# Kernel tuning notes

Hardware: AMD Instinct MI355X
Metric: run time of the kernel (lower is better)

## Reference

```python
import jax, jax.numpy as jnp
import numpy as np

B, L, H = 32, 4096, 512


def setup_inputs() -> dict:
    key = jax.random.key(0)
    k1, k2, k3, k4 = jax.random.split(key, 4)
    hidden = jax.random.normal(k1, (2, 2, B, H), dtype=jnp.float32)  # (h/c, layers, batch, H)
    encoder_outputs = jax.random.normal(k2, (B, L, H), dtype=jnp.float32)
    W = jax.random.normal(k3, (H, H), dtype=jnp.float32) * (1.0 / np.sqrt(H))
    b = jax.random.normal(k4, (H,), dtype=jnp.float32) * 0.02
    return {"hidden": hidden, "encoder_outputs": encoder_outputs, "W": W, "b": b}


def reference(hidden, encoder_outputs, W, b):
    # hidden[0]: h-state [layers, batch, H] -> transpose(0,1) -> [batch, layers, H] -> last layer
    h_last = hidden[0].transpose(1, 0, 2)[:, -1, :]            # [B, H]
    # method == 'general': energy[b,i] = h_last[b] . (W @ enc[b,i] + b)
    proj = jnp.einsum('blh,oh->blo', encoder_outputs, W) + b   # [B, L, H]
    energies = jnp.einsum('bh,blh->bl', h_last, proj)          # [B, L]
    return jax.nn.softmax(energies, axis=1)[:, None, :]        # [B, 1, L]
```

## Files before the change

kernel.cpp:

```cpp
#include <hip/hip_runtime.h>

#define BATCH 32
#define LSEQ 4096
#define HDIM 512

typedef float f32x4 __attribute__((ext_vector_type(4)));

__global__ __launch_bounds__(512) void proj_kernel(
    const float* __restrict__ hidden, const float* __restrict__ W,
    const float* __restrict__ bias, float* __restrict__ vpart,
    float* __restrict__ cpart)
{
    const int b    = blockIdx.x;
    const int part = blockIdx.y;
    const int h    = threadIdx.x;
    const int obase = part * (HDIM / 2);

    __shared__ float s_hl[HDIM / 2];
    if (h < HDIM / 2) s_hl[h] = hidden[(BATCH + b) * HDIM + obase + h];
    __syncthreads();

    float acc = 0.f;
#pragma unroll 16
    for (int o = 0; o < HDIM / 2; ++o) {
        acc += s_hl[o] * W[(obase + o) * HDIM + h];
    }
    vpart[(part * BATCH + b) * HDIM + h] = acc;

    float p = (h < HDIM / 2) ? s_hl[h] * bias[obase + h] : 0.f;
#pragma unroll
    for (int off = 1; off < 64; off <<= 1) p += __shfl_xor(p, off, 64);

    __shared__ float red[8];
    const int wid  = h >> 6;
    const int lane = h & 63;
    if (lane == 0) red[wid] = p;
    __syncthreads();
    if (h == 0) {
        float s = 0.f;
#pragma unroll
        for (int w = 0; w < 8; ++w) s += red[w];
        cpart[part * BATCH + b] = s;
    }
}

__global__ __launch_bounds__(256) void energy_kernel(
    const float* __restrict__ enc, const float* __restrict__ vA,
    const float* __restrict__ vB, const float* __restrict__ cA,
    const float* __restrict__ cB, float* __restrict__ energies)
{
    const int wave = threadIdx.x >> 6;
    const int lane = threadIdx.x & 63;
    const long r0 = (long)blockIdx.x * 16 + wave * 4;
    const int b = (int)(r0 >> 12);

    const f32x4* e4 = (const f32x4*)(enc + r0 * HDIM) + lane * 2;
    const float4* va = (const float4*)(vA + (long)b * HDIM) + lane * 2;
    const float4* vb = (const float4*)(vB + (long)b * HDIM) + lane * 2;

    f32x4 e[8];
#pragma unroll
    for (int j = 0; j < 4; ++j) {
        e[2 * j]     = __builtin_nontemporal_load(e4 + j * 128);
        e[2 * j + 1] = __builtin_nontemporal_load(e4 + j * 128 + 1);
    }
    float4 v0 = va[0], v1 = va[1];
    const float4 w0 = vb[0], w1 = vb[1];
    v0.x += w0.x; v0.y += w0.y; v0.z += w0.z; v0.w += w0.w;
    v1.x += w1.x; v1.y += w1.y; v1.z += w1.z; v1.w += w1.w;

    float d[4];
#pragma unroll
    for (int j = 0; j < 4; ++j) {
        const f32x4 a = e[2 * j], c = e[2 * j + 1];
        d[j] = a.x * v0.x + a.y * v0.y + a.z * v0.z + a.w * v0.w
             + c.x * v1.x + c.y * v1.y + c.z * v1.z + c.w * v1.w;
    }

#pragma unroll
    for (int off = 1; off < 64; off <<= 1) {
#pragma unroll
        for (int j = 0; j < 4; ++j) d[j] += __shfl_xor(d[j], off, 64);
    }

    if (lane == 0) {
        const float cb = cA[b] + cB[b];
        float4 out = { d[0] + cb, d[1] + cb, d[2] + cb, d[3] + cb };
        *(float4*)(energies + r0) = out;
    }
}

__global__ __launch_bounds__(512) void softmax_kernel(float* __restrict__ out)
{
    const int b = blockIdx.x;
    const int t = threadIdx.x;
    const int wid  = t >> 6;
    const int lane = t & 63;

    float4* o4 = (float4*)(out + (long)b * LSEQ);

    float4 v0 = o4[t], v1 = o4[512 + t];
    float m = fmaxf(fmaxf(fmaxf(v0.x, v0.y), fmaxf(v0.z, v0.w)),
                    fmaxf(fmaxf(v1.x, v1.y), fmaxf(v1.z, v1.w)));

    __shared__ float smax[8];
#pragma unroll
    for (int off = 1; off < 64; off <<= 1) m = fmaxf(m, __shfl_xor(m, off, 64));
    if (lane == 0) smax[wid] = m;
    __syncthreads();
#pragma unroll
    for (int w = 0; w < 8; ++w) m = fmaxf(m, smax[w]);

    v0.x = __expf(v0.x - m); v0.y = __expf(v0.y - m);
    v0.z = __expf(v0.z - m); v0.w = __expf(v0.w - m);
    v1.x = __expf(v1.x - m); v1.y = __expf(v1.y - m);
    v1.z = __expf(v1.z - m); v1.w = __expf(v1.w - m);

    float s = v0.x + v0.y + v0.z + v0.w + v1.x + v1.y + v1.z + v1.w;
    __shared__ float ssum[8];
#pragma unroll
    for (int off = 1; off < 64; off <<= 1) s += __shfl_xor(s, off, 64);
    if (lane == 0) ssum[wid] = s;
    __syncthreads();
    s = 0.f;
#pragma unroll
    for (int w = 0; w < 8; ++w) s += ssum[w];

    const float inv = 1.0f / s;
    v0.x *= inv; v0.y *= inv; v0.z *= inv; v0.w *= inv;
    v1.x *= inv; v1.y *= inv; v1.z *= inv; v1.w *= inv;
    o4[t] = v0;
    o4[512 + t] = v1;
}

extern "C" void kernel_launch(void* const* d_in, const int* in_sizes, int n_in,
                              void* d_out, int out_size, void* d_ws, size_t ws_size,
                              hipStream_t stream)
{
    const float* hidden = (const float*)d_in[0];
    const float* enc    = (const float*)d_in[1];
    const float* W      = (const float*)d_in[2];
    const float* bias   = (const float*)d_in[3];

    float* ws    = (float*)d_ws;
    float* vpart = ws;
    float* cpart = ws + 2 * BATCH * HDIM;

    float* out = (float*)d_out;

    proj_kernel<<<dim3(BATCH, 2), 512, 0, stream>>>(hidden, W, bias, vpart, cpart);
    energy_kernel<<<(BATCH * LSEQ) / 16, 256, 0, stream>>>(
        enc, vpart, vpart + BATCH * HDIM, cpart, cpart + BATCH, out);
    softmax_kernel<<<BATCH, 512, 0, stream>>>(out);
}
```

Measured before the change: 61.29 us.

## Split projection into four parts and restructure energy kernel with per-row subgroups

The projection kernel now splits the output dimension into four parts instead of two, giving more blocks and a shorter serial loop per thread. The energy kernel is restructured so each wave handles 32 rows, with 16-lane subgroups per row, a 4-step shuffle reduction, and the projected vector loaded once per thread and reused across rows. The softmax uses 1024 threads with one float4 each. The aim is to cut redundant vector loads and long shuffle chains in the bandwidth-bound energy pass, at the cost of fewer blocks in flight and scalar output stores.

```diff
diff --git a/kernel.cpp b/kernel.cpp
--- a/kernel.cpp
+++ b/kernel.cpp
@@ -3,6 +3,7 @@
 #define BATCH 32
 #define LSEQ 4096
 #define HDIM 512
+#define PARTS 4
 
 typedef float f32x4 __attribute__((ext_vector_type(4)));
 
@@ -14,20 +15,21 @@
     const int b    = blockIdx.x;
     const int part = blockIdx.y;
     const int h    = threadIdx.x;
-    const int obase = part * (HDIM / 2);
+    const int OS   = HDIM / PARTS;
+    const int obase = part * OS;
 
-    __shared__ float s_hl[HDIM / 2];
-    if (h < HDIM / 2) s_hl[h] = hidden[(BATCH + b) * HDIM + obase + h];
+    __shared__ float s_hl[HDIM / PARTS];
+    if (h < OS) s_hl[h] = hidden[(BATCH + b) * HDIM + obase + h];
     __syncthreads();
 
     float acc = 0.f;
 #pragma unroll 16
-    for (int o = 0; o < HDIM / 2; ++o) {
+    for (int o = 0; o < OS; ++o) {
         acc += s_hl[o] * W[(obase + o) * HDIM + h];
     }
     vpart[(part * BATCH + b) * HDIM + h] = acc;
 
-    float p = (h < HDIM / 2) ? s_hl[h] * bias[obase + h] : 0.f;
+    float p = (h < OS) ? s_hl[h] * bias[obase + h] : 0.f;
 #pragma unroll
     for (int off = 1; off < 64; off <<= 1) p += __shfl_xor(p, off, 64);
 
@@ -45,52 +47,59 @@
 }
 
 __global__ __launch_bounds__(256) void energy_kernel(
-    const float* __restrict__ enc, const float* __restrict__ vA,
-    const float* __restrict__ vB, const float* __restrict__ cA,
-    const float* __restrict__ cB, float* __restrict__ energies)
+    const float* __restrict__ enc, const float* __restrict__ vpart,
+    const float* __restrict__ cpart, float* __restrict__ energies)
 {
     const int wave = threadIdx.x >> 6;
     const int lane = threadIdx.x & 63;
-    const long r0 = (long)blockIdx.x * 16 + wave * 4;
-    const int b = (int)(r0 >> 12);
+    const int sub  = lane >> 4;
+    const int sl   = lane & 15;
 
-    const f32x4* e4 = (const f32x4*)(enc + r0 * HDIM) + lane * 2;
-    const float4* va = (const float4*)(vA + (long)b * HDIM) + lane * 2;
-    const float4* vb = (const float4*)(vB + (long)b * HDIM) + lane * 2;
+    const int b      = blockIdx.x >> 5;
+    const int l_base = (blockIdx.x & 31) * 128 + wave * 32;
 
-    f32x4 e[8];
+    const f32x4* vp0 = (const f32x4*)(vpart + (0 * BATCH + b) * HDIM);
+    const f32x4* vp1 = (const f32x4*)(vpart + (1 * BATCH + b) * HDIM);
+    const f32x4* vp2 = (const f32x4*)(vpart + (2 * BATCH + b) * HDIM);
+    const f32x4* vp3 = (const f32x4*)(vpart + (3 * BATCH + b) * HDIM);
+    f32x4 vv[8];
 #pragma unroll
-    for (int j = 0; j < 4; ++j) {
-        e[2 * j]     = __builtin_nontemporal_load(e4 + j * 128);
-        e[2 * j + 1] = __builtin_nontemporal_load(e4 + j * 128 + 1);
+    for (int k = 0; k < 8; ++k) {
+        const int ch = sl + 16 * k;
+        vv[k] = vp0[ch] + vp1[ch] + vp2[ch] + vp3[ch];
     }
-    float4 v0 = va[0], v1 = va[1];
-    const float4 w0 = vb[0], w1 = vb[1];
-    v0.x += w0.x; v0.y += w0.y; v0.z += w0.z; v0.w += w0.w;
-    v1.x += w1.x; v1.y += w1.y; v1.z += w1.z; v1.w += w1.w;
+    const float cb = cpart[b] + cpart[BATCH + b] + cpart[2 * BATCH + b]
+                   + cpart[3 * BATCH + b];
 
-    float d[4];
+    const long rbase = (long)b * LSEQ + l_base;
+
+#pragma unroll 2
+    for (int batch = 0; batch < 8; ++batch) {
+        const long r = rbase + batch * 4 + sub;
+        const f32x4* ep = (const f32x4*)(enc + r * HDIM) + sl;
+
+        f32x4 e[8];
 #pragma unroll
-    for (int j = 0; j < 4; ++j) {
-        const f32x4 a = e[2 * j], c = e[2 * j + 1];
-        d[j] = a.x * v0.x + a.y * v0.y + a.z * v0.z + a.w * v0.w
-             + c.x * v1.x + c.y * v1.y + c.z * v1.z + c.w * v1.w;
-    }
+        for (int k = 0; k < 8; ++k)
+            e[k] = __builtin_nontemporal_load(ep + 16 * k);
 
+        float d = 0.f;
 #pragma unroll
-    for (int off = 1; off < 64; off <<= 1) {
-#pragma unroll
-        for (int j = 0; j < 4; ++j) d[j] += __shfl_xor(d[j], off, 64);
-    }
+        for (int k = 0; k < 8; ++k) {
+            d += e[k].x * vv[k].x + e[k].y * vv[k].y
+               + e[k].z * vv[k].z + e[k].w * vv[k].w;
+        }
 
-    if (lane == 0) {
-        const float cb = cA[b] + cB[b];
-        float4 out = { d[0] + cb, d[1] + cb, d[2] + cb, d[3] + cb };
-        *(float4*)(energies + r0) = out;
+        d += __shfl_xor(d, 1, 64);
+        d += __shfl_xor(d, 2, 64);
+        d += __shfl_xor(d, 4, 64);
+        d += __shfl_xor(d, 8, 64);
+
+        if (sl == 0) energies[r] = d + cb;
     }
 }
 
-__global__ __launch_bounds__(512) void softmax_kernel(float* __restrict__ out)
+__global__ __launch_bounds__(1024) void softmax_kernel(float* __restrict__ out)
 {
     const int b = blockIdx.x;
     const int t = threadIdx.x;
@@ -99,38 +108,33 @@
 
     float4* o4 = (float4*)(out + (long)b * LSEQ);
 
-    float4 v0 = o4[t], v1 = o4[512 + t];
-    float m = fmaxf(fmaxf(fmaxf(v0.x, v0.y), fmaxf(v0.z, v0.w)),
-                    fmaxf(fmaxf(v1.x, v1.y), fmaxf(v1.z, v1.w)));
+    float4 v0 = o4[t];
+    float m = fmaxf(fmaxf(v0.x, v0.y), fmaxf(v0.z, v0.w));
 
-    __shared__ float smax[8];
+    __shared__ float smax[16];
 #pragma unroll
     for (int off = 1; off < 64; off <<= 1) m = fmaxf(m, __shfl_xor(m, off, 64));
     if (lane == 0) smax[wid] = m;
     __syncthreads();
 #pragma unroll
-    for (int w = 0; w < 8; ++w) m = fmaxf(m, smax[w]);
+    for (int w = 0; w < 16; ++w) m = fmaxf(m, smax[w]);
 
     v0.x = __expf(v0.x - m); v0.y = __expf(v0.y - m);
     v0.z = __expf(v0.z - m); v0.w = __expf(v0.w - m);
-    v1.x = __expf(v1.x - m); v1.y = __expf(v1.y - m);
-    v1.z = __expf(v1.z - m); v1.w = __expf(v1.w - m);
 
-    float s = v0.x + v0.y + v0.z + v0.w + v1.x + v1.y + v1.z + v1.w;
-    __shared__ float ssum[8];
+    float s = v0.x + v0.y + v0.z + v0.w;
+    __shared__ float ssum[16];
 #pragma unroll
     for (int off = 1; off < 64; off <<= 1) s += __shfl_xor(s, off, 64);
     if (lane == 0) ssum[wid] = s;
     __syncthreads();
     s = 0.f;
 #pragma unroll
-    for (int w = 0; w < 8; ++w) s += ssum[w];
+    for (int w = 0; w < 16; ++w) s += ssum[w];
 
     const float inv = 1.0f / s;
     v0.x *= inv; v0.y *= inv; v0.z *= inv; v0.w *= inv;
-    v1.x *= inv; v1.y *= inv; v1.z *= inv; v1.w *= inv;
     o4[t] = v0;
-    o4[512 + t] = v1;
 }
 
 extern "C" void kernel_launch(void* const* d_in, const int* in_sizes, int n_in,
@@ -144,12 +148,11 @@
 
     float* ws    = (float*)d_ws;
     float* vpart = ws;
-    float* cpart = ws + 2 * BATCH * HDIM;
+    float* cpart = ws + PARTS * BATCH * HDIM;
 
     float* out = (float*)d_out;
 
-    proj_kernel<<<dim3(BATCH, 2), 512, 0, stream>>>(hidden, W, bias, vpart, cpart);
-    energy_kernel<<<(BATCH * LSEQ) / 16, 256, 0, stream>>>(
-        enc, vpart, vpart + BATCH * HDIM, cpart, cpart + BATCH, out);
-    softmax_kernel<<<BATCH, 512, 0, stream>>>(out);
+    proj_kernel<<<dim3(BATCH, PARTS), 512, 0, stream>>>(hidden, W, bias, vpart, cpart);
+    energy_kernel<<<(BATCH * LSEQ) / 128, 256, 0, stream>>>(enc, vpart, cpart, out);
+    softmax_kernel<<<BATCH, 1024, 0, stream>>>(out);
 }
```

Result: faster. 57.92 us (-5.5%).
